# Kernel optimization log

Measured on AMD Instinct MI355X. Metric: run time of the kernel, lower is better.

## Reference

```python
import jax, jax.numpy as jnp
import numpy as np

N_NODES = 50000
N_EDGES = 800000
NODE = 128
EDGE = 16
H = 96
OUT = 64
L = 3
BN_EPS = 1e-5


def setup_inputs() -> dict:
    key = jax.random.key(0)
    ks = iter(jax.random.split(key, 48))
    def rn(shape, s=0.05):
        return jax.random.normal(next(ks), shape, dtype=jnp.float32) * s
    inp = {
        "x": jax.random.normal(next(ks), (N_NODES, NODE), dtype=jnp.float32),
        "edge_index": jax.random.randint(next(ks), (2, N_EDGES), 0, N_NODES, dtype=jnp.int32),
        "edge_attr": jax.random.normal(next(ks), (N_EDGES, EDGE), dtype=jnp.float32),
        # GCNConv (layer 0)
        "gcn_lin_w": rn((NODE, H)), "gcn_lin_b": rn((H,)),
        "gcn_root": rn((1, H)),
        "gcn_bw1": rn((EDGE, H)), "gcn_bb1": rn((H,)),
        "gcn_bw2": rn((H, H)), "gcn_bb2": rn((H,)),
        # GINConv layers 1..L-1 (stacked)
        "gin_bw1": rn((L - 1, EDGE, H)), "gin_bb1": rn((L - 1, H)),
        "gin_bw2": rn((L - 1, H, H)), "gin_bb2": rn((L - 1, H)),
        "gin_mw1": rn((L - 1, H, H)), "gin_mb1": rn((L - 1, H)),
        "gin_mw2": rn((L - 1, H, H)), "gin_mb2": rn((L - 1, H)),
        "gin_eps": jnp.zeros((L - 1,), jnp.float32),
        # BatchNorm (eval mode, running stats)
        "bn_gamma": jnp.ones((L, H), jnp.float32),
        "bn_beta": jnp.zeros((L, H), jnp.float32),
        "bn_mean": rn((L, H)),
        "bn_var": jnp.ones((L, H), jnp.float32) + jax.random.uniform(next(ks), (L, H), dtype=jnp.float32) * 0.1,
        # head
        "fc1_w": rn((L * H, H)), "fc1_b": rn((H,)),
        "fc2_w": rn((H, OUT)), "fc2_b": rn((OUT,)),
    }
    return inp


def _bn(x, gamma, beta, mean, var):
    return (x - mean) * jax.lax.rsqrt(var + BN_EPS) * gamma + beta


def reference(x, edge_index, edge_attr,
              gcn_lin_w, gcn_lin_b, gcn_root, gcn_bw1, gcn_bb1, gcn_bw2, gcn_bb2,
              gin_bw1, gin_bb1, gin_bw2, gin_bb2, gin_mw1, gin_mb1, gin_mw2, gin_mb2, gin_eps,
              bn_gamma, bn_beta, bn_mean, bn_var,
              fc1_w, fc1_b, fc2_w, fc2_b):
    n = x.shape[0]
    row, col = edge_index[0], edge_index[1]  # source, target

    # ---- Layer 0: GCNConv with edge attributes ----
    h = x @ gcn_lin_w + gcn_lin_b                                    # [N,H]
    ee = jax.nn.relu(edge_attr @ gcn_bw1 + gcn_bb1) @ gcn_bw2 + gcn_bb2  # [E,H]
    deg = jax.ops.segment_sum(jnp.ones_like(row, dtype=h.dtype), row, num_segments=n) + 1.0
    dinv = jax.lax.rsqrt(deg)                                        # deg >= 1, no inf
    norm = dinv[row] * dinv[col]                                     # [E]
    msg = norm[:, None] * jax.nn.relu(h[row] + ee)                   # [E,H]
    agg = jax.ops.segment_sum(msg, col, num_segments=n)              # [N,H]
    h = agg + jax.nn.relu(h + gcn_root) / deg[:, None]
    h = _bn(jax.nn.relu(h), bn_gamma[0], bn_beta[0], bn_mean[0], bn_var[0])
    feats = [h]

    # ---- Layers 1..L-1: GINConv with edge attributes ----
    for i in range(L - 1):
        ee = jax.nn.relu(edge_attr @ gin_bw1[i] + gin_bb1[i]) @ gin_bw2[i] + gin_bb2[i]  # [E,H]
        agg = jax.ops.segment_sum(jax.nn.relu(h[row] + ee), col, num_segments=n)          # [N,H]
        z = (1.0 + gin_eps[i]) * h + agg
        z = jax.nn.relu(z @ gin_mw1[i] + gin_mb1[i]) @ gin_mw2[i] + gin_mb2[i]
        h = _bn(jax.nn.relu(z), bn_gamma[i + 1], bn_beta[i + 1], bn_mean[i + 1], bn_var[i + 1])
        feats.append(h)

    cat = jnp.concatenate(feats, axis=-1)                            # [N, L*H]
    y = jax.nn.relu(cat @ fc1_w + fc1_b)                             # dropout is eval-mode identity
    return y @ fc2_w + fc2_b                                         # [N, OUT]
```

## Files before the change

kernel.cpp:

```cpp
#include <hip/hip_runtime.h>
#include <hip/hip_bf16.h>


#define HH 96
#define EDGEF 16
#define CAT (3 * HH)

typedef __attribute__((ext_vector_type(8))) short bf16x8;
typedef __attribute__((ext_vector_type(4))) float f32x4;
typedef __attribute__((ext_vector_type(4))) unsigned short ubf16x4;
typedef __attribute__((ext_vector_type(2))) unsigned uint2v;

typedef union { bf16x8 v; unsigned u[4]; } bfpack8;
typedef union { ubf16x4 v; unsigned u[2]; } bfpack4;

__device__ __forceinline__ unsigned short f2bf(float f) {
    unsigned u = __float_as_uint(f);
    u += 0x7fffu + ((u >> 16) & 1u);
    return (unsigned short)(u >> 16);
}
__device__ __forceinline__ float bf2f(unsigned short s) {
    return __uint_as_float(((unsigned)s) << 16);
}
__device__ __forceinline__ unsigned pkbf2(float lo, float hi) {
    __hip_bfloat162 b = __float22bfloat162_rn(make_float2(lo, hi));
    union { __hip_bfloat162 b2; unsigned u; } cv; cv.b2 = b; return cv.u;
}

template <int K, int F, int AMODE, int EPI>
__global__ __launch_bounds__(256) void node_gemm(
    const void* __restrict__ Aptr, int lda,
    const float* __restrict__ W, const float* __restrict__ bias,
    void* __restrict__ Cptr, int ldc,
    unsigned short* __restrict__ bf_copy,
    int M)
{
    constexpr int SW = ((K * 2) % 128 == 0) ? 7 : 3;
    constexpr int NFT = F / 16;
    __shared__ __align__(16) short s_wt[F * K];

    const int tid = threadIdx.x;
    const int lane = tid & 63;
    const int w = tid >> 6;
    const int lr = lane & 15;
    const int lg = lane >> 4;

    for (int idx = tid; idx < F * K; idx += 256) {
        int f = idx / K, k = idx - f * K;
        s_wt[idx ^ ((f & SW) << 3)] = (short)f2bf(W[k * F + f]);
    }
    __syncthreads();

    const int R0 = blockIdx.x * 64 + 16 * w;
    const int Ra = min(R0 + lr, M - 1);

    f32x4 acc[NFT];
#pragma unroll
    for (int ft = 0; ft < NFT; ++ft) {
        float b = bias[16 * ft + lr];
        acc[ft][0] = b; acc[ft][1] = b; acc[ft][2] = b; acc[ft][3] = b;
    }

#pragma unroll
    for (int kt = 0; kt < K / 32; ++kt) {
        bf16x8 ae;
        if (AMODE == 0) {
            const float* ap = (const float*)Aptr + (size_t)Ra * lda + 32 * kt + 8 * lg;
            f32x4 a0 = *(const f32x4*)ap;
            f32x4 a1 = *(const f32x4*)(ap + 4);
            bfpack8 p;
            p.u[0] = pkbf2(a0[0], a0[1]); p.u[1] = pkbf2(a0[2], a0[3]);
            p.u[2] = pkbf2(a1[0], a1[1]); p.u[3] = pkbf2(a1[2], a1[3]);
            ae = p.v;
        } else {
            ae = *(const bf16x8*)((const unsigned short*)Aptr + (size_t)Ra * lda + 32 * kt + 8 * lg);
        }
#pragma unroll
        for (int ft = 0; ft < NFT; ++ft) {
            bf16x8 bw = *(const bf16x8*)&s_wt[((lr + 16 * ft) * K + 32 * kt + 8 * lg) ^ ((lr & SW) << 3)];
            acc[ft] = __builtin_amdgcn_mfma_f32_16x16x32_bf16(ae, bw, acc[ft], 0, 0, 0);
        }
    }

#pragma unroll
    for (int reg = 0; reg < 4; ++reg) {
        int r = R0 + 4 * lg + reg;
        if (r < M) {
#pragma unroll
            for (int ft = 0; ft < NFT; ++ft) {
                int col = 16 * ft + lr;
                float v = acc[ft][reg];
                if (EPI == 0) {
                    ((float*)Cptr)[(size_t)r * ldc + col] = v;
                } else if (EPI == 1) {
                    ((unsigned short*)Cptr)[(size_t)r * ldc + col] = f2bf(fmaxf(v, 0.f));
                } else {
                    ((float*)Cptr)[(size_t)r * ldc + col] = v;
                    bf_copy[(size_t)r * F + col] = f2bf(v);
                }
            }
        }
    }
}

__global__ __launch_bounds__(256) void gin_mlp(
    const unsigned short* __restrict__ hb_in,
    const float* __restrict__ agg,
    const float* __restrict__ eps_arr, int li,
    const float* __restrict__ mw1, const float* __restrict__ mb1,
    const float* __restrict__ mw2, const float* __restrict__ mb2,
    const float* __restrict__ gamma, const float* __restrict__ beta,
    const float* __restrict__ mean, const float* __restrict__ var,
    unsigned short* __restrict__ featsbf, int slot,
    unsigned short* __restrict__ hb_out,
    int M)
{
    __shared__ __align__(16) short s_w1t[96][104];
    __shared__ __align__(16) short s_w2t[96][104];
    __shared__ __align__(16) short s_z[4][16][104];
    __shared__ float s_b[192];

    const int tid = threadIdx.x;
    const int lane = tid & 63;
    const int w = tid >> 6;
    const int lr = lane & 15;
    const int lg = lane >> 4;

    for (int idx = tid; idx < HH * HH; idx += 256) {
        int k = idx / HH, f = idx - k * HH;
        s_w1t[f][k] = (short)f2bf(mw1[idx]);
        s_w2t[f][k] = (short)f2bf(mw2[idx]);
    }
    if (tid < HH) { s_b[tid] = mb1[tid]; s_b[HH + tid] = mb2[tid]; }
    __syncthreads();

    const int R0 = blockIdx.x * 64 + 16 * w;
    const int Ra = min(R0 + lr, M - 1);
    const float e1 = 1.f + eps_arr[li];

    bf16x8 inf[3];
#pragma unroll
    for (int kt = 0; kt < 3; ++kt) {
        const unsigned short* hp = hb_in + (size_t)Ra * HH + 32 * kt + 8 * lg;
        bf16x8 h8 = *(const bf16x8*)hp;
        const float* gp = agg + (size_t)Ra * HH + 32 * kt + 8 * lg;
        f32x4 g0 = *(const f32x4*)gp;
        f32x4 g1 = *(const f32x4*)(gp + 4);
        float t0 = fmaf(e1, bf2f((unsigned short)h8[0]), g0[0]);
        float t1 = fmaf(e1, bf2f((unsigned short)h8[1]), g0[1]);
        float t2 = fmaf(e1, bf2f((unsigned short)h8[2]), g0[2]);
        float t3 = fmaf(e1, bf2f((unsigned short)h8[3]), g0[3]);
        float t4 = fmaf(e1, bf2f((unsigned short)h8[4]), g1[0]);
        float t5 = fmaf(e1, bf2f((unsigned short)h8[5]), g1[1]);
        float t6 = fmaf(e1, bf2f((unsigned short)h8[6]), g1[2]);
        float t7 = fmaf(e1, bf2f((unsigned short)h8[7]), g1[3]);
        bfpack8 p;
        p.u[0] = pkbf2(t0, t1); p.u[1] = pkbf2(t2, t3);
        p.u[2] = pkbf2(t4, t5); p.u[3] = pkbf2(t6, t7);
        inf[kt] = p.v;
    }

#pragma unroll
    for (int ft = 0; ft < 6; ++ft) {
        f32x4 t4v = *(const f32x4*)&s_b[16 * ft + 4 * lg];
#pragma unroll
        for (int kt = 0; kt < 3; ++kt) {
            bf16x8 aw = *(const bf16x8*)&s_w1t[16 * ft + lr][32 * kt + 8 * lg];
            t4v = __builtin_amdgcn_mfma_f32_16x16x32_bf16(aw, inf[kt], t4v, 0, 0, 0);
        }
        uint2v uu;
        uu[0] = pkbf2(fmaxf(t4v[0], 0.f), fmaxf(t4v[1], 0.f));
        uu[1] = pkbf2(fmaxf(t4v[2], 0.f), fmaxf(t4v[3], 0.f));
        *(uint2v*)&s_z[w][lr][16 * ft + 4 * lg] = uu;
    }
    __builtin_amdgcn_wave_barrier();

    bf16x8 az[3];
#pragma unroll
    for (int kt = 0; kt < 3; ++kt)
        az[kt] = *(const bf16x8*)&s_z[w][lr][32 * kt + 8 * lg];

    f32x4 acc[6];
#pragma unroll
    for (int ft = 0; ft < 6; ++ft) {
        float b = s_b[HH + 16 * ft + lr];
        acc[ft][0] = b; acc[ft][1] = b; acc[ft][2] = b; acc[ft][3] = b;
#pragma unroll
        for (int kt = 0; kt < 3; ++kt) {
            bf16x8 bw = *(const bf16x8*)&s_w2t[16 * ft + lr][32 * kt + 8 * lg];
            acc[ft] = __builtin_amdgcn_mfma_f32_16x16x32_bf16(az[kt], bw, acc[ft], 0, 0, 0);
        }
    }

    float scale[6], shiftv[6];
#pragma unroll
    for (int ft = 0; ft < 6; ++ft) {
        int col = 16 * ft + lr;
        float s = gamma[col] * rsqrtf(var[col] + 1e-5f);
        scale[ft] = s;
        shiftv[ft] = beta[col] - mean[col] * s;
    }
#pragma unroll
    for (int reg = 0; reg < 4; ++reg) {
        int r = R0 + 4 * lg + reg;
        if (r < M) {
#pragma unroll
            for (int ft = 0; ft < 6; ++ft) {
                int col = 16 * ft + lr;
                float z = fmaxf(acc[ft][reg], 0.f) * scale[ft] + shiftv[ft];
                unsigned short zb = f2bf(z);
                featsbf[(size_t)r * CAT + slot * HH + col] = zb;
                hb_out[(size_t)r * HH + col] = zb;
            }
        }
    }
}

__global__ void init_kernel(float* __restrict__ deg, int* __restrict__ cnt, int N)
{
    int i = blockIdx.x * blockDim.x + threadIdx.x;
    if (i < N) { deg[i] = 1.f; cnt[i] = 0; }
}

__global__ void count_kernel(const int* __restrict__ row, const int* __restrict__ col,
                             float* __restrict__ deg, int* __restrict__ cnt, int E)
{
    int e = blockIdx.x * blockDim.x + threadIdx.x;
    if (e < E) {
        atomicAdd(&deg[row[e]], 1.f);
        atomicAdd(&cnt[col[e]], 1);
    }
}

__global__ void scan1_kernel(const int* __restrict__ cnt, int* __restrict__ start,
                             int* __restrict__ bsum, int N)
{
    __shared__ int s[256];
    int tid = threadIdx.x;
    int i = blockIdx.x * 256 + tid;
    int v = (i < N) ? cnt[i] : 0;
    s[tid] = v;
    __syncthreads();
#pragma unroll
    for (int off = 1; off < 256; off <<= 1) {
        int t = (tid >= off) ? s[tid - off] : 0;
        __syncthreads();
        s[tid] += t;
        __syncthreads();
    }
    if (i < N) start[i] = s[tid] - v;
    if (tid == 255) bsum[blockIdx.x] = s[255];
}

__global__ void scan2_kernel(int* __restrict__ bsum, int nb)
{
    __shared__ int s[256];
    int tid = threadIdx.x;
    int v = (tid < nb) ? bsum[tid] : 0;
    s[tid] = v;
    __syncthreads();
#pragma unroll
    for (int off = 1; off < 256; off <<= 1) {
        int t = (tid >= off) ? s[tid - off] : 0;
        __syncthreads();
        s[tid] += t;
        __syncthreads();
    }
    if (tid < nb) bsum[tid] = s[tid] - v;
}

__global__ void scan3_kernel(int* __restrict__ start, const int* __restrict__ bsum,
                             int* __restrict__ cursor,
                             const float* __restrict__ deg, float* __restrict__ dinv,
                             int N, int E)
{
    int i = blockIdx.x * blockDim.x + threadIdx.x;
    if (i < N) {
        int f = start[i] + bsum[i >> 8];
        start[i] = f;
        cursor[i] = f;
        dinv[i] = rsqrtf(deg[i]);
    } else if (i == N) {
        start[N] = E;
    }
}

__global__ void scatter_ea_kernel(const int* __restrict__ row, const int* __restrict__ col,
                                  int* __restrict__ cursor,
                                  const float* __restrict__ ea,
                                  int* __restrict__ row_sorted,
                                  unsigned short* __restrict__ eas, int E)
{
    int e = blockIdx.x * blockDim.x + threadIdx.x;
    if (e >= E) return;
    int c = col[e];
    int p = atomicAdd(&cursor[c], 1);
    row_sorted[p] = row[e];
    const float* src = ea + (size_t)e * EDGEF;
    f32x4 v0 = *(const f32x4*)(src);
    f32x4 v1 = *(const f32x4*)(src + 4);
    f32x4 v2 = *(const f32x4*)(src + 8);
    f32x4 v3 = *(const f32x4*)(src + 12);
    bfpack8 o0, o1;
    o0.u[0] = pkbf2(v0[0], v0[1]); o0.u[1] = pkbf2(v0[2], v0[3]);
    o0.u[2] = pkbf2(v1[0], v1[1]); o0.u[3] = pkbf2(v1[2], v1[3]);
    o1.u[0] = pkbf2(v2[0], v2[1]); o1.u[1] = pkbf2(v2[2], v2[3]);
    o1.u[2] = pkbf2(v3[0], v3[1]); o1.u[3] = pkbf2(v3[2], v3[3]);
    *(bf16x8*)(eas + (size_t)p * EDGEF) = o0.v;
    *(bf16x8*)(eas + (size_t)p * EDGEF + 8) = o1.v;
}

template <bool GCN>
__global__ __launch_bounds__(256, 4) void edge_kernel(
    const unsigned short* __restrict__ ea_sorted,
    const int* __restrict__ row_sorted,
    const int* __restrict__ seg_start,
    const float* __restrict__ bw1, const float* __restrict__ bb1,
    const float* __restrict__ bw2, const float* __restrict__ bb2,
    const unsigned short* __restrict__ hbf,
    const float* __restrict__ dinv,
    float* __restrict__ agg,
    int N)
{
    __shared__ __align__(16) short s_bw2T[96][104];
    __shared__ __align__(16) short s_bw1T[96][16];
    __shared__ __align__(16) short s_t[4][16][104];
    __shared__ float s_bias[192];

    const int tid = threadIdx.x;
    const int lane = tid & 63;
    const int w = tid >> 6;
    const int lr = lane & 15;
    const int lg = lane >> 4;

    for (int idx = tid; idx < HH * HH; idx += 256) {
        int k = idx / HH, f = idx - k * HH;
        s_bw2T[f][k] = (short)f2bf(bw2[idx]);
    }
    for (int idx = tid; idx < EDGEF * HH; idx += 256) {
        int k = idx / HH, f = idx - k * HH;
        s_bw1T[f][k] = (short)f2bf(bw1[idx]);
    }
    if (tid < HH) { s_bias[tid] = bb1[tid]; s_bias[HH + tid] = bb2[tid]; }
    __syncthreads();

    bf16x8 bwf[6];
#pragma unroll
    for (int ft = 0; ft < 6; ++ft) {
        bf16x8 z;
#pragma unroll
        for (int j = 0; j < 8; ++j) z[j] = 0;
        if (lg < 2) z = *(const bf16x8*)&s_bw1T[lr + 16 * ft][8 * lg];
        bwf[ft] = z;
    }

    const int nwaves = gridDim.x * 4;

    for (int c = blockIdx.x * 4 + w; c < N; c += nwaves) {
        const int s0 = seg_start[c];
        const int s1 = seg_start[c + 1];
        const float dinv_c = GCN ? dinv[c] : 1.f;

        f32x4 acc[6];
#pragma unroll
        for (int ft = 0; ft < 6; ++ft) { acc[ft][0]=0.f; acc[ft][1]=0.f; acc[ft][2]=0.f; acc[ft][3]=0.f; }

        for (int b = s0; b < s1; b += 16) {
            const int epos = b + lr;
            const bool vld = (epos < s1);
            const int epc = vld ? epos : s0;
            const int r = row_sorted[epc];

            const unsigned short* hrow = hbf + (size_t)r * HH + 4 * lg;
            ubf16x4 hv[6];
#pragma unroll
            for (int ft = 0; ft < 6; ++ft)
                hv[ft] = *(const ubf16x4*)(hrow + 16 * ft);

            const float msk = vld ? (GCN ? dinv[r] * dinv_c : 1.f) : 0.f;

            bf16x8 ae = *(const bf16x8*)(ea_sorted + (size_t)epc * EDGEF + 8 * (lg & 1));

#pragma unroll
            for (int ft = 0; ft < 6; ++ft) {
                f32x4 ci = *(const f32x4*)&s_bias[16 * ft + 4 * lg];
                f32x4 t4 = __builtin_amdgcn_mfma_f32_16x16x32_bf16(bwf[ft], ae, ci, 0, 0, 0);
                uint2v uu;
                uu[0] = pkbf2(fmaxf(t4[0], 0.f), fmaxf(t4[1], 0.f));
                uu[1] = pkbf2(fmaxf(t4[2], 0.f), fmaxf(t4[3], 0.f));
                *(uint2v*)&s_t[w][lr][16 * ft + 4 * lg] = uu;
            }
            __builtin_amdgcn_wave_barrier();

            bf16x8 bt[3];
#pragma unroll
            for (int kt = 0; kt < 3; ++kt)
                bt[kt] = *(const bf16x8*)&s_t[w][lr][8 * lg + 32 * kt];

#pragma unroll
            for (int ft = 0; ft < 6; ++ft) {
                const int fb = 16 * ft + 4 * lg;
                f32x4 ee = *(const f32x4*)&s_bias[HH + fb];
#pragma unroll
                for (int kt = 0; kt < 3; ++kt) {
                    bf16x8 aw = *(const bf16x8*)&s_bw2T[lr + 16 * ft][8 * lg + 32 * kt];
                    ee = __builtin_amdgcn_mfma_f32_16x16x32_bf16(aw, bt[kt], ee, 0, 0, 0);
                }
#pragma unroll
                for (int reg = 0; reg < 4; ++reg) {
                    float m = fmaxf(bf2f(hv[ft][reg]) + ee[reg], 0.f);
                    acc[ft][reg] = fmaf(m, msk, acc[ft][reg]);
                }
            }
        }

#pragma unroll
        for (int ft = 0; ft < 6; ++ft) {
#pragma unroll
            for (int reg = 0; reg < 4; ++reg) {
                float v = acc[ft][reg];
                v += __shfl_xor(v, 1);
                v += __shfl_xor(v, 2);
                v += __shfl_xor(v, 4);
                v += __shfl_xor(v, 8);
                acc[ft][reg] = v;
            }
        }
        if (lr == 0) {
#pragma unroll
            for (int ft = 0; ft < 6; ++ft)
                *(f32x4*)&agg[(size_t)c * HH + 16 * ft + 4 * lg] = acc[ft];
        }
    }
}

__global__ void gcn_epilogue_kernel(
    const float* __restrict__ agg, const float* __restrict__ hbuf,
    const float* __restrict__ root, const float* __restrict__ deg,
    const float* __restrict__ gamma, const float* __restrict__ beta,
    const float* __restrict__ mean, const float* __restrict__ var,
    unsigned short* __restrict__ featsbf, unsigned short* __restrict__ hb, int N)
{
    int idx = blockIdx.x * blockDim.x + threadIdx.x;
    if (idx >= N * (HH / 4)) return;
    int n = idx / (HH / 4), q = idx - n * (HH / 4);
    int f0 = 4 * q;
    f32x4 a  = *(const f32x4*)&agg[(size_t)n * HH + f0];
    f32x4 h  = *(const f32x4*)&hbuf[(size_t)n * HH + f0];
    f32x4 rt = *(const f32x4*)&root[f0];
    f32x4 gm = *(const f32x4*)&gamma[f0];
    f32x4 bt = *(const f32x4*)&beta[f0];
    f32x4 mn = *(const f32x4*)&mean[f0];
    f32x4 vr = *(const f32x4*)&var[f0];
    float di = 1.f / deg[n];
    float vv[4];
#pragma unroll
    for (int j = 0; j < 4; ++j) {
        float self = fmaxf(h[j] + rt[j], 0.f) * di;
        float v = fmaxf(a[j] + self, 0.f);
        vv[j] = (v - mn[j]) * rsqrtf(vr[j] + 1e-5f) * gm[j] + bt[j];
    }
    bfpack4 o;
    o.u[0] = pkbf2(vv[0], vv[1]);
    o.u[1] = pkbf2(vv[2], vv[3]);
    *(ubf16x4*)&featsbf[(size_t)n * CAT + f0] = o.v;
    *(ubf16x4*)&hb[(size_t)n * HH + f0] = o.v;
}

extern "C" void kernel_launch(void* const* d_in, const int* in_sizes, int n_in,
                              void* d_out, int out_size, void* d_ws, size_t ws_size,
                              hipStream_t stream)
{
    const float* x         = (const float*)d_in[0];
    const int*   eidx      = (const int*)d_in[1];
    const float* edge_attr = (const float*)d_in[2];
    const float* gcn_lin_w = (const float*)d_in[3];
    const float* gcn_lin_b = (const float*)d_in[4];
    const float* gcn_root  = (const float*)d_in[5];
    const float* gcn_bw1   = (const float*)d_in[6];
    const float* gcn_bb1   = (const float*)d_in[7];
    const float* gcn_bw2   = (const float*)d_in[8];
    const float* gcn_bb2   = (const float*)d_in[9];
    const float* gin_bw1   = (const float*)d_in[10];
    const float* gin_bb1   = (const float*)d_in[11];
    const float* gin_bw2   = (const float*)d_in[12];
    const float* gin_bb2   = (const float*)d_in[13];
    const float* gin_mw1   = (const float*)d_in[14];
    const float* gin_mb1   = (const float*)d_in[15];
    const float* gin_mw2   = (const float*)d_in[16];
    const float* gin_mb2   = (const float*)d_in[17];
    const float* gin_eps   = (const float*)d_in[18];
    const float* bn_gamma  = (const float*)d_in[19];
    const float* bn_beta   = (const float*)d_in[20];
    const float* bn_mean   = (const float*)d_in[21];
    const float* bn_var    = (const float*)d_in[22];
    const float* fc1_w     = (const float*)d_in[23];
    const float* fc1_b     = (const float*)d_in[24];
    const float* fc2_w     = (const float*)d_in[25];
    const float* fc2_b     = (const float*)d_in[26];
    float* out = (float*)d_out;

    const int N = in_sizes[0] / 128;
    const int E = in_sizes[1] / 2;
    const int* row = eidx;
    const int* col = eidx + E;

    char* ws = (char*)d_ws;
    float* deg        = (float*)(ws);
    float* dinv       = (float*)(ws + (size_t)256 * 1024);
    int*   seg_start  = (int*)(ws + (size_t)512 * 1024);
    int*   cursor     = (int*)(ws + (size_t)768 * 1024);
    int*   bsum       = (int*)(ws + (size_t)1024 * 1024);
    int*   row_sorted = (int*)(ws + (size_t)1088 * 1024);
    unsigned short* ea_sorted = (unsigned short*)(ws + (size_t)8 * 1024 * 1024);
    unsigned short* hb        = (unsigned short*)(ws + (size_t)34 * 1024 * 1024);
    float* hbuf   = (float*)(ws + (size_t)44 * 1024 * 1024);
    float* agg    = (float*)(ws + (size_t)64 * 1024 * 1024);
    unsigned short* featsbf = (unsigned short*)(ws + (size_t)84 * 1024 * 1024);
    unsigned short* r1bf    = (unsigned short*)(ws + (size_t)123 * 1024 * 1024);

    const int ew_blocks = 1024;
    const int q_grid = (N * (HH / 4) + 255) / 256;
    const int gemm_grid = (N + 63) / 64;
    const int e_grid = (E + 255) / 256;
    const int n_grid = (N + 255) / 256;
    const int nchunks = (N + 255) / 256;

    init_kernel<<<n_grid, 256, 0, stream>>>(deg, cursor, N);
    count_kernel<<<e_grid, 256, 0, stream>>>(row, col, deg, cursor, E);
    scan1_kernel<<<nchunks, 256, 0, stream>>>(cursor, seg_start, bsum, N);
    scan2_kernel<<<1, 256, 0, stream>>>(bsum, nchunks);
    scan3_kernel<<<(N + 256) / 256, 256, 0, stream>>>(seg_start, bsum, cursor, deg, dinv, N, E);
    scatter_ea_kernel<<<e_grid, 256, 0, stream>>>(row, col, cursor, edge_attr,
                                                  row_sorted, ea_sorted, E);

    node_gemm<128, 96, 0, 3><<<gemm_grid, 256, 0, stream>>>(
        x, 128, gcn_lin_w, gcn_lin_b, hbuf, HH, hb, N);
    edge_kernel<true><<<ew_blocks, 256, 0, stream>>>(
        ea_sorted, row_sorted, seg_start,
        gcn_bw1, gcn_bb1, gcn_bw2, gcn_bb2, hb, dinv, agg, N);
    gcn_epilogue_kernel<<<q_grid, 256, 0, stream>>>(
        agg, hbuf, gcn_root, deg, bn_gamma, bn_beta, bn_mean, bn_var, featsbf, hb, N);

    for (int i = 0; i < 2; ++i) {
        edge_kernel<false><<<ew_blocks, 256, 0, stream>>>(
            ea_sorted, row_sorted, seg_start,
            gin_bw1 + (size_t)i * EDGEF * HH, gin_bb1 + i * HH,
            gin_bw2 + (size_t)i * HH * HH, gin_bb2 + i * HH,
            hb, dinv, agg, N);
        gin_mlp<<<gemm_grid, 256, 0, stream>>>(
            hb, agg, gin_eps, i,
            gin_mw1 + (size_t)i * HH * HH, gin_mb1 + i * HH,
            gin_mw2 + (size_t)i * HH * HH, gin_mb2 + i * HH,
            bn_gamma + (i + 1) * HH, bn_beta + (i + 1) * HH,
            bn_mean + (i + 1) * HH, bn_var + (i + 1) * HH,
            featsbf, i + 1, hb, N);
    }

    node_gemm<288, 96, 1, 1><<<gemm_grid, 256, 0, stream>>>(
        featsbf, CAT, fc1_w, fc1_b, r1bf, HH, nullptr, N);
    node_gemm<96, 64, 1, 0><<<gemm_grid, 256, 0, stream>>>(
        r1bf, HH, fc2_w, fc2_b, out, 64, nullptr, N);
}
```

Before: 597.4 us.

## Pre-swizzle edge-kernel LDS into fragment order and prefetch next edge batch

The bw2 weights and the per-wave intermediate tile in LDS are now stored in MFMA fragment order, so each lane reads a contiguous 16-byte chunk. This is meant to avoid bank conflicts and the padded layout. bw1 fragments are loaded straight from global memory into registers, which drops one LDS array. The row index and edge attributes for the next 16-edge batch are software-prefetched to hide gather latency, and the grid grows from 1024 to 1280 blocks. In exchange, register pressure rises, and the prefetch near the segment end reads a clamped, redundant index.

```diff
diff --git a/kernel.cpp b/kernel.cpp
--- a/kernel.cpp
+++ b/kernel.cpp
@@ -322,9 +322,8 @@
     float* __restrict__ agg,
     int N)
 {
-    __shared__ __align__(16) short s_bw2T[96][104];
-    __shared__ __align__(16) short s_bw1T[96][16];
-    __shared__ __align__(16) short s_t[4][16][104];
+    __shared__ __align__(16) short s_bw2F[96 * 96];
+    __shared__ __align__(16) short s_tF[4][16 * 96];
     __shared__ float s_bias[192];
 
     const int tid = threadIdx.x;
@@ -334,15 +333,16 @@
     const int lg = lane >> 4;
 
     for (int idx = tid; idx < HH * HH; idx += 256) {
-        int k = idx / HH, f = idx - k * HH;
-        s_bw2T[f][k] = (short)f2bf(bw2[idx]);
-    }
-    for (int idx = tid; idx < EDGEF * HH; idx += 256) {
-        int k = idx / HH, f = idx - k * HH;
-        s_bw1T[f][k] = (short)f2bf(bw1[idx]);
+        int j = idx & 7;
+        int plr = (idx >> 3) & 15;
+        int frag = idx >> 7;
+        int plg = frag & 3;
+        int rem = frag >> 2;
+        int pkt = rem % 3;
+        int pft = rem / 3;
+        s_bw2F[idx] = (short)f2bf(bw2[(8 * plg + 32 * pkt + j) * HH + plr + 16 * pft]);
     }
     if (tid < HH) { s_bias[tid] = bb1[tid]; s_bias[HH + tid] = bb2[tid]; }
-    __syncthreads();
 
     bf16x8 bwf[6];
 #pragma unroll
@@ -350,9 +350,14 @@
         bf16x8 z;
 #pragma unroll
         for (int j = 0; j < 8; ++j) z[j] = 0;
-        if (lg < 2) z = *(const bf16x8*)&s_bw1T[lr + 16 * ft][8 * lg];
+        if (lg < 2) {
+#pragma unroll
+            for (int j = 0; j < 8; ++j)
+                z[j] = (short)f2bf(bw1[(8 * lg + j) * HH + lr + 16 * ft]);
+        }
         bwf[ft] = z;
     }
+    __syncthreads();
 
     const int nwaves = gridDim.x * 4;
 
@@ -365,11 +370,13 @@
 #pragma unroll
         for (int ft = 0; ft < 6; ++ft) { acc[ft][0]=0.f; acc[ft][1]=0.f; acc[ft][2]=0.f; acc[ft][3]=0.f; }
 
+        bool vld = (s0 + lr) < s1;
+        int ep = vld ? (s0 + lr) : s0;
+        int r = row_sorted[ep];
+        bf16x8 ae = *(const bf16x8*)(ea_sorted + (size_t)ep * EDGEF + 8 * (lg & 1));
+
         for (int b = s0; b < s1; b += 16) {
-            const int epos = b + lr;
-            const bool vld = (epos < s1);
-            const int epc = vld ? epos : s0;
-            const int r = row_sorted[epc];
+            const float msk = vld ? (GCN ? dinv[r] * dinv_c : 1.f) : 0.f;
 
             const unsigned short* hrow = hbf + (size_t)r * HH + 4 * lg;
             ubf16x4 hv[6];
@@ -377,9 +384,11 @@
             for (int ft = 0; ft < 6; ++ft)
                 hv[ft] = *(const ubf16x4*)(hrow + 16 * ft);
 
-            const float msk = vld ? (GCN ? dinv[r] * dinv_c : 1.f) : 0.f;
-
-            bf16x8 ae = *(const bf16x8*)(ea_sorted + (size_t)epc * EDGEF + 8 * (lg & 1));
+            const int bn = b + 16;
+            const bool vldn = (bn + lr) < s1;
+            const int epn = vldn ? (bn + lr) : s0;
+            const int rn = row_sorted[epn];
+            bf16x8 aen = *(const bf16x8*)(ea_sorted + (size_t)epn * EDGEF + 8 * (lg & 1));
 
 #pragma unroll
             for (int ft = 0; ft < 6; ++ft) {
@@ -388,14 +397,16 @@
                 uint2v uu;
                 uu[0] = pkbf2(fmaxf(t4[0], 0.f), fmaxf(t4[1], 0.f));
                 uu[1] = pkbf2(fmaxf(t4[2], 0.f), fmaxf(t4[3], 0.f));
-                *(uint2v*)&s_t[w][lr][16 * ft + 4 * lg] = uu;
+                const int ktw = ft >> 1;
+                const int lgw = ((ft & 1) << 1) + (lg >> 1);
+                *(uint2v*)&s_tF[w][((ktw * 4 + lgw) * 16 + lr) * 8 + 4 * (lg & 1)] = uu;
             }
             __builtin_amdgcn_wave_barrier();
 
             bf16x8 bt[3];
 #pragma unroll
             for (int kt = 0; kt < 3; ++kt)
-                bt[kt] = *(const bf16x8*)&s_t[w][lr][8 * lg + 32 * kt];
+                bt[kt] = *(const bf16x8*)&s_tF[w][((kt * 4 + lg) * 16 + lr) * 8];
 
 #pragma unroll
             for (int ft = 0; ft < 6; ++ft) {
@@ -403,7 +414,7 @@
                 f32x4 ee = *(const f32x4*)&s_bias[HH + fb];
 #pragma unroll
                 for (int kt = 0; kt < 3; ++kt) {
-                    bf16x8 aw = *(const bf16x8*)&s_bw2T[lr + 16 * ft][8 * lg + 32 * kt];
+                    bf16x8 aw = *(const bf16x8*)&s_bw2F[(((ft * 3 + kt) * 4 + lg) * 16 + lr) * 8];
                     ee = __builtin_amdgcn_mfma_f32_16x16x32_bf16(aw, bt[kt], ee, 0, 0, 0);
                 }
 #pragma unroll
@@ -412,6 +423,8 @@
                     acc[ft][reg] = fmaf(m, msk, acc[ft][reg]);
                 }
             }
+
+            vld = vldn; r = rn; ae = aen;
         }
 
 #pragma unroll
@@ -519,7 +532,7 @@
     unsigned short* featsbf = (unsigned short*)(ws + (size_t)84 * 1024 * 1024);
     unsigned short* r1bf    = (unsigned short*)(ws + (size_t)123 * 1024 * 1024);
 
-    const int ew_blocks = 1024;
+    const int ew_blocks = 1280;
     const int q_grid = (N * (HH / 4) + 255) / 256;
     const int gemm_grid = (N + 63) / 64;
     const int e_grid = (E + 255) / 256;
```

Result: slower. 619.0 us (+3.6%).

## Process two destination nodes per wave to overlap gathers and MFMA work

Applied to the files above, without the earlier changes.

Each wave now handles a pair of destination nodes and interleaves their edge batches, issuing both sets of gathers before either set of MFMAs. This adds instruction-level parallelism and hides gather latency. The bw1 weights now go straight from global memory into registers, with no shared staging. Launch bounds drop to 3 waves per SIMD to make room for the doubled register state, which lowers occupancy. With an odd N, the last pair sets cB equal to cA, so that node's row is computed twice and written twice with the same value.

```diff
diff --git a/kernel.cpp b/kernel.cpp
--- a/kernel.cpp
+++ b/kernel.cpp
@@ -311,7 +311,7 @@
 }
 
 template <bool GCN>
-__global__ __launch_bounds__(256, 4) void edge_kernel(
+__global__ __launch_bounds__(256, 3) void edge_kernel(
     const unsigned short* __restrict__ ea_sorted,
     const int* __restrict__ row_sorted,
     const int* __restrict__ seg_start,
@@ -323,8 +323,7 @@
     int N)
 {
     __shared__ __align__(16) short s_bw2T[96][104];
-    __shared__ __align__(16) short s_bw1T[96][16];
-    __shared__ __align__(16) short s_t[4][16][104];
+    __shared__ __align__(16) short s_t[4][2][16][104];
     __shared__ float s_bias[192];
 
     const int tid = threadIdx.x;
@@ -337,12 +336,7 @@
         int k = idx / HH, f = idx - k * HH;
         s_bw2T[f][k] = (short)f2bf(bw2[idx]);
     }
-    for (int idx = tid; idx < EDGEF * HH; idx += 256) {
-        int k = idx / HH, f = idx - k * HH;
-        s_bw1T[f][k] = (short)f2bf(bw1[idx]);
-    }
     if (tid < HH) { s_bias[tid] = bb1[tid]; s_bias[HH + tid] = bb2[tid]; }
-    __syncthreads();
 
     bf16x8 bwf[6];
 #pragma unroll
@@ -350,86 +344,161 @@
         bf16x8 z;
 #pragma unroll
         for (int j = 0; j < 8; ++j) z[j] = 0;
-        if (lg < 2) z = *(const bf16x8*)&s_bw1T[lr + 16 * ft][8 * lg];
+        if (lg < 2) {
+#pragma unroll
+            for (int j = 0; j < 8; ++j)
+                z[j] = (short)f2bf(bw1[(8 * lg + j) * HH + lr + 16 * ft]);
+        }
         bwf[ft] = z;
     }
+    __syncthreads();
 
     const int nwaves = gridDim.x * 4;
 
-    for (int c = blockIdx.x * 4 + w; c < N; c += nwaves) {
-        const int s0 = seg_start[c];
-        const int s1 = seg_start[c + 1];
-        const float dinv_c = GCN ? dinv[c] : 1.f;
-
-        f32x4 acc[6];
-#pragma unroll
-        for (int ft = 0; ft < 6; ++ft) { acc[ft][0]=0.f; acc[ft][1]=0.f; acc[ft][2]=0.f; acc[ft][3]=0.f; }
-
-        for (int b = s0; b < s1; b += 16) {
-            const int epos = b + lr;
-            const bool vld = (epos < s1);
-            const int epc = vld ? epos : s0;
-            const int r = row_sorted[epc];
-
-            const unsigned short* hrow = hbf + (size_t)r * HH + 4 * lg;
-            ubf16x4 hv[6];
-#pragma unroll
-            for (int ft = 0; ft < 6; ++ft)
-                hv[ft] = *(const ubf16x4*)(hrow + 16 * ft);
-
-            const float msk = vld ? (GCN ? dinv[r] * dinv_c : 1.f) : 0.f;
-
-            bf16x8 ae = *(const bf16x8*)(ea_sorted + (size_t)epc * EDGEF + 8 * (lg & 1));
-
+    for (int p = blockIdx.x * 4 + w; 2 * p < N; p += nwaves) {
+        const int cA = 2 * p;
+        const int cB = min(2 * p + 1, N - 1);
+        const int s0A = seg_start[cA], s1A = seg_start[cA + 1];
+        const int s0B = seg_start[cB], s1B = seg_start[cB + 1];
+        const float dcA = GCN ? dinv[cA] : 1.f;
+        const float dcB = GCN ? dinv[cB] : 1.f;
+
+        f32x4 accA[6], accB[6];
+#pragma unroll
+        for (int ft = 0; ft < 6; ++ft) {
+            accA[ft][0]=0.f; accA[ft][1]=0.f; accA[ft][2]=0.f; accA[ft][3]=0.f;
+            accB[ft][0]=0.f; accB[ft][1]=0.f; accB[ft][2]=0.f; accB[ft][3]=0.f;
+        }
+
+        int bA = s0A, bB = s0B;
+        while (bA < s1A || bB < s1B) {
+            const bool doA = bA < s1A;
+            const bool doB = bB < s1B;
+
+            ubf16x4 hvA[6], hvB[6];
+            bf16x8 aeA, aeB;
+            float mskA = 0.f, mskB = 0.f;
+            if (doA) {
+                const int ep = bA + lr;
+                const bool v = ep < s1A;
+                const int ec = v ? ep : s0A;
+                const int r = row_sorted[ec];
+                const unsigned short* hrow = hbf + (size_t)r * HH + 4 * lg;
+#pragma unroll
+                for (int ft = 0; ft < 6; ++ft) hvA[ft] = *(const ubf16x4*)(hrow + 16 * ft);
+                mskA = v ? (GCN ? dinv[r] * dcA : 1.f) : 0.f;
+                aeA = *(const bf16x8*)(ea_sorted + (size_t)ec * EDGEF + 8 * (lg & 1));
+            }
+            if (doB) {
+                const int ep = bB + lr;
+                const bool v = ep < s1B;
+                const int ec = v ? ep : s0B;
+                const int r = row_sorted[ec];
+                const unsigned short* hrow = hbf + (size_t)r * HH + 4 * lg;
+#pragma unroll
+                for (int ft = 0; ft < 6; ++ft) hvB[ft] = *(const ubf16x4*)(hrow + 16 * ft);
+                mskB = v ? (GCN ? dinv[r] * dcB : 1.f) : 0.f;
+                aeB = *(const bf16x8*)(ea_sorted + (size_t)ec * EDGEF + 8 * (lg & 1));
+            }
+
+            if (doA) {
+#pragma unroll
+                for (int ft = 0; ft < 6; ++ft) {
+                    f32x4 ci = *(const f32x4*)&s_bias[16 * ft + 4 * lg];
+                    f32x4 t4 = __builtin_amdgcn_mfma_f32_16x16x32_bf16(bwf[ft], aeA, ci, 0, 0, 0);
+                    uint2v uu;
+                    uu[0] = pkbf2(fmaxf(t4[0], 0.f), fmaxf(t4[1], 0.f));
+                    uu[1] = pkbf2(fmaxf(t4[2], 0.f), fmaxf(t4[3], 0.f));
+                    *(uint2v*)&s_t[w][0][lr][16 * ft + 4 * lg] = uu;
+                }
+            }
+            if (doB) {
+#pragma unroll
+                for (int ft = 0; ft < 6; ++ft) {
+                    f32x4 ci = *(const f32x4*)&s_bias[16 * ft + 4 * lg];
+                    f32x4 t4 = __builtin_amdgcn_mfma_f32_16x16x32_bf16(bwf[ft], aeB, ci, 0, 0, 0);
+                    uint2v uu;
+                    uu[0] = pkbf2(fmaxf(t4[0], 0.f), fmaxf(t4[1], 0.f));
+                    uu[1] = pkbf2(fmaxf(t4[2], 0.f), fmaxf(t4[3], 0.f));
+                    *(uint2v*)&s_t[w][1][lr][16 * ft + 4 * lg] = uu;
+                }
+            }
+            __builtin_amdgcn_wave_barrier();
+
+            bf16x8 btA[3], btB[3];
+            if (doA) {
+#pragma unroll
+                for (int kt = 0; kt < 3; ++kt)
+                    btA[kt] = *(const bf16x8*)&s_t[w][0][lr][8 * lg + 32 * kt];
+            }
+            if (doB) {
+#pragma unroll
+                for (int kt = 0; kt < 3; ++kt)
+                    btB[kt] = *(const bf16x8*)&s_t[w][1][lr][8 * lg + 32 * kt];
+            }
+
+            if (doA) {
+#pragma unroll
+                for (int ft = 0; ft < 6; ++ft) {
+                    const int fb = 16 * ft + 4 * lg;
+                    f32x4 ee = *(const f32x4*)&s_bias[HH + fb];
+#pragma unroll
+                    for (int kt = 0; kt < 3; ++kt) {
+                        bf16x8 aw = *(const bf16x8*)&s_bw2T[lr + 16 * ft][8 * lg + 32 * kt];
+                        ee = __builtin_amdgcn_mfma_f32_16x16x32_bf16(aw, btA[kt], ee, 0, 0, 0);
+                    }
+#pragma unroll
+                    for (int reg = 0; reg < 4; ++reg) {
+                        float m = fmaxf(bf2f(hvA[ft][reg]) + ee[reg], 0.f);
+                        accA[ft][reg] = fmaf(m, mskA, accA[ft][reg]);
+                    }
+                }
+            }
+            if (doB) {
+#pragma unroll
+                for (int ft = 0; ft < 6; ++ft) {
+                    const int fb = 16 * ft + 4 * lg;
+                    f32x4 ee = *(const f32x4*)&s_bias[HH + fb];
+#pragma unroll
+                    for (int kt = 0; kt < 3; ++kt) {
+                        bf16x8 aw = *(const bf16x8*)&s_bw2T[lr + 16 * ft][8 * lg + 32 * kt];
+                        ee = __builtin_amdgcn_mfma_f32_16x16x32_bf16(aw, btB[kt], ee, 0, 0, 0);
+                    }
+#pragma unroll
+                    for (int reg = 0; reg < 4; ++reg) {
+                        float m = fmaxf(bf2f(hvB[ft][reg]) + ee[reg], 0.f);
+                        accB[ft][reg] = fmaf(m, mskB, accB[ft][reg]);
+                    }
+                }
+            }
+
+            bA += 16; bB += 16;
+        }
+
+#pragma unroll
+        for (int ft = 0; ft < 6; ++ft) {
+#pragma unroll
+            for (int reg = 0; reg < 4; ++reg) {
+                float vA = accA[ft][reg];
+                vA += __shfl_xor(vA, 1);
+                vA += __shfl_xor(vA, 2);
+                vA += __shfl_xor(vA, 4);
+                vA += __shfl_xor(vA, 8);
+                accA[ft][reg] = vA;
+                float vB = accB[ft][reg];
+                vB += __shfl_xor(vB, 1);
+                vB += __shfl_xor(vB, 2);
+                vB += __shfl_xor(vB, 4);
+                vB += __shfl_xor(vB, 8);
+                accB[ft][reg] = vB;
+            }
+        }
+        if (lr == 0) {
 #pragma unroll
             for (int ft = 0; ft < 6; ++ft) {
-                f32x4 ci = *(const f32x4*)&s_bias[16 * ft + 4 * lg];
-                f32x4 t4 = __builtin_amdgcn_mfma_f32_16x16x32_bf16(bwf[ft], ae, ci, 0, 0, 0);
-                uint2v uu;
-                uu[0] = pkbf2(fmaxf(t4[0], 0.f), fmaxf(t4[1], 0.f));
-                uu[1] = pkbf2(fmaxf(t4[2], 0.f), fmaxf(t4[3], 0.f));
-                *(uint2v*)&s_t[w][lr][16 * ft + 4 * lg] = uu;
-            }
-            __builtin_amdgcn_wave_barrier();
-
-            bf16x8 bt[3];
-#pragma unroll
-            for (int kt = 0; kt < 3; ++kt)
-                bt[kt] = *(const bf16x8*)&s_t[w][lr][8 * lg + 32 * kt];
-
-#pragma unroll
-            for (int ft = 0; ft < 6; ++ft) {
-                const int fb = 16 * ft + 4 * lg;
-                f32x4 ee = *(const f32x4*)&s_bias[HH + fb];
-#pragma unroll
-                for (int kt = 0; kt < 3; ++kt) {
-                    bf16x8 aw = *(const bf16x8*)&s_bw2T[lr + 16 * ft][8 * lg + 32 * kt];
-                    ee = __builtin_amdgcn_mfma_f32_16x16x32_bf16(aw, bt[kt], ee, 0, 0, 0);
-                }
-#pragma unroll
-                for (int reg = 0; reg < 4; ++reg) {
-                    float m = fmaxf(bf2f(hv[ft][reg]) + ee[reg], 0.f);
-                    acc[ft][reg] = fmaf(m, msk, acc[ft][reg]);
-                }
-            }
-        }
-
-#pragma unroll
-        for (int ft = 0; ft < 6; ++ft) {
-#pragma unroll
-            for (int reg = 0; reg < 4; ++reg) {
-                float v = acc[ft][reg];
-                v += __shfl_xor(v, 1);
-                v += __shfl_xor(v, 2);
-                v += __shfl_xor(v, 4);
-                v += __shfl_xor(v, 8);
-                acc[ft][reg] = v;
-            }
-        }
-        if (lr == 0) {
-#pragma unroll
-            for (int ft = 0; ft < 6; ++ft)
-                *(f32x4*)&agg[(size_t)c * HH + 16 * ft + 4 * lg] = acc[ft];
+                *(f32x4*)&agg[(size_t)cA * HH + 16 * ft + 4 * lg] = accA[ft];
+                *(f32x4*)&agg[(size_t)cB * HH + 16 * ft + 4 * lg] = accB[ft];
+            }
         }
     }
 }
```

Measured after the change: 772.3 us. +29.3%, slower.
